# Performance work log

Hardware: AMD Instinct MI355X
Metric: run time of the kernel (lower is better)

The kernel has to match this reference:

```python
import jax, jax.numpy as jnp
import numpy as np

B, F, N = 8, 32, 512
H = 8  # nb_hidden

def setup_inputs() -> dict:
    key = jax.random.key(0)
    ks = jax.random.split(key, 6)
    return {
        "adj_in": jax.random.uniform(ks[0], (B, N, N), dtype=jnp.float32),
        "emb_in": jax.random.normal(ks[1], (B, F, N), dtype=jnp.float32),
        "W1": jax.random.normal(ks[2], (2 * F + 1, H), dtype=jnp.float32) * 0.1,
        "b1": jax.random.normal(ks[3], (H,), dtype=jnp.float32) * 0.1,
        "W2": jax.random.normal(ks[4], (H, 1), dtype=jnp.float32) * 0.1,
        "b2": jax.random.normal(ks[5], (1,), dtype=jnp.float32) * 0.1,
    }

def reference(adj_in, emb_in, W1, b1, W2, b2):
    b_, f_, n_ = emb_in.shape
    # Faithful to the torch code's .resize quirk: column sums always come from
    # batch 0, while the subtracted diagonal is per-batch.
    col_sum0 = adj_in[0].sum(axis=0)                      # [N] = sum_k adj_in[0,k,j]
    diag = jnp.diagonal(adj_in, axis1=1, axis2=2)          # [B,N]
    sw = (col_sum0[None, :] - diag) / (n_ - 1)             # [B,N]
    et = jnp.transpose(emb_in, (0, 2, 1))                  # [B,N,F]
    a = jnp.broadcast_to(et[:, :, None, :], (b_, n_, n_, f_))   # src node i feats
    c = jnp.broadcast_to(et[:, None, :, :], (b_, n_, n_, f_))   # dst node j feats
    swb = jnp.broadcast_to(sw[:, None, :, None], (b_, n_, n_, 1))  # sw[j]
    feat = jnp.concatenate([a, c, swb], axis=-1)           # [B,N,N,2F+1]
    h = jax.nn.relu(feat @ W1 + b1)                        # [B,N,N,H]
    out = (h @ W2 + b2)[..., 0]                            # [B,N,N]
    return jax.nn.sigmoid(out)
```

## Files before the change

### kernel.cpp

```cpp
#include <hip/hip_runtime.h>
#include <math.h>

constexpr int NB = 8;
constexpr int NF = 32;
constexpr int NN = 512;
constexpr int NH = 8;
constexpr int JC = 32;
constexpr int IR = 256;

__global__ __launch_bounds__(512) void fused1_kernel(
    const float* __restrict__ adj, const float* __restrict__ emb,
    const float* __restrict__ W1, const float* __restrict__ b1,
    const float* __restrict__ W2, const float* __restrict__ b2,
    float* __restrict__ out)
{
    __shared__ float u_lds[NH][IR];
    __shared__ float v_lds[NH][JC];
    __shared__ float cs_lds[8][JC];

    const int jc = blockIdx.x;
    const int ih = blockIdx.y;
    const int b  = blockIdx.z;
    const int j0 = jc * JC;
    const int i0 = ih * IR;
    const int t  = threadIdx.x;

    if (t < 256) {
        const int i = i0 + t;
        float uo[NH];
        #pragma unroll
        for (int k = 0; k < NH; ++k) uo[k] = 0.f;
        #pragma unroll 8
        for (int f = 0; f < NF; ++f) {
            const float e = emb[((size_t)b * NF + f) * NN + i];
            #pragma unroll
            for (int k = 0; k < NH; ++k)
                uo[k] = fmaf(e, W1[f * NH + k], uo[k]);
        }
        #pragma unroll
        for (int k = 0; k < NH; ++k) u_lds[k][t] = uo[k];
    } else {
        const int tt = t - 256;
        const int c  = tt & 31;
        const int rg = tt >> 5;
        const float* p = adj + (size_t)(rg * 64) * NN + j0 + c;
        float acc = 0.f;
        #pragma unroll 16
        for (int r = 0; r < 64; ++r)
            acc += p[(size_t)r * NN];
        cs_lds[rg][c] = acc;
    }
    __syncthreads();

    if (t >= 256 && t < 256 + JC) {
        const int c = t - 256;
        const int n = j0 + c;
        float cs = 0.f;
        #pragma unroll
        for (int rg = 0; rg < 8; ++rg) cs += cs_lds[rg][c];
        const float dg = adj[((size_t)b * NN + n) * NN + n];
        const float sw = (cs - dg) * (1.0f / (float)(NN - 1));

        float vo[NH];
        #pragma unroll
        for (int k = 0; k < NH; ++k)
            vo[k] = b1[k] + sw * W1[2 * NF * NH + k];
        #pragma unroll 8
        for (int f = 0; f < NF; ++f) {
            const float e = emb[((size_t)b * NF + f) * NN + n];
            #pragma unroll
            for (int k = 0; k < NH; ++k)
                vo[k] = fmaf(e, W1[(NF + f) * NH + k], vo[k]);
        }
        #pragma unroll
        for (int k = 0; k < NH; ++k) v_lds[k][c] = vo[k];
    }
    __syncthreads();

    float w2[NH];
    #pragma unroll
    for (int k = 0; k < NH; ++k) w2[k] = W2[k];
    const float bias = b2[0];

    const int j    = t & 31;
    const int isub = t >> 5;

    float vv[NH];
    #pragma unroll
    for (int k = 0; k < NH; ++k) vv[k] = v_lds[k][j];

    float* orow = out + ((size_t)b * NN + i0) * NN + j0 + j;
    #pragma unroll 4
    for (int r = 0; r < 16; ++r) {
        const int i = isub * 16 + r;
        float a = bias;
        #pragma unroll
        for (int k = 0; k < NH; ++k)
            a = fmaf(fmaxf(u_lds[k][i] + vv[k], 0.f), w2[k], a);
        orow[(size_t)i * NN] = 1.0f / (1.0f + __expf(-a));
    }
}

extern "C" void kernel_launch(void* const* d_in, const int* in_sizes, int n_in,
                              void* d_out, int out_size, void* d_ws, size_t ws_size,
                              hipStream_t stream) {
    const float* adj = (const float*)d_in[0];
    const float* emb = (const float*)d_in[1];
    const float* W1  = (const float*)d_in[2];
    const float* b1  = (const float*)d_in[3];
    const float* W2  = (const float*)d_in[4];
    const float* b2  = (const float*)d_in[5];
    float* out = (float*)d_out;

    fused1_kernel<<<dim3(NN / JC, NN / IR, NB), 512, 0, stream>>>(
        adj, emb, W1, b1, W2, b2, out);
}
```

Before: 11.84 us.

## Vectorize column-sum loads and output stores with float4, use fast reciprocal

The column-sum phase now has each thread load float4 chunks over 16 rows instead of scalar loads over 64 rows, and keeps 32 partial float4 sums in LDS. The output phase gives each thread 4 consecutive columns and 4 rows, writes float4 stores, and computes the sigmoid with a hardware reciprocal instead of a division. The aim is fewer, wider memory transactions for both the adjacency read and the output write, plus a cheaper sigmoid. The cost is a longer LDS reduction over 32 partials with a select per element, and the fast reciprocal is slightly less accurate.

```diff
diff --git a/kernel.cpp b/kernel.cpp
--- a/kernel.cpp
+++ b/kernel.cpp
@@ -14,9 +14,9 @@
     const float* __restrict__ W2, const float* __restrict__ b2,
     float* __restrict__ out)
 {
-    __shared__ float u_lds[NH][IR];
-    __shared__ float v_lds[NH][JC];
-    __shared__ float cs_lds[8][JC];
+    __shared__ float  u_lds[NH][IR];
+    __shared__ float  v_lds[NH][JC];
+    __shared__ float4 cs_lds[32][8];
 
     const int jc = blockIdx.x;
     const int ih = blockIdx.y;
@@ -41,14 +41,17 @@
         for (int k = 0; k < NH; ++k) u_lds[k][t] = uo[k];
     } else {
         const int tt = t - 256;
-        const int c  = tt & 31;
-        const int rg = tt >> 5;
-        const float* p = adj + (size_t)(rg * 64) * NN + j0 + c;
-        float acc = 0.f;
+        const int c4 = tt & 7;
+        const int rg = tt >> 3;
+        const float4* p = reinterpret_cast<const float4*>(
+            adj + (size_t)(rg * 16) * NN + j0 + c4 * 4);
+        float4 acc = make_float4(0.f, 0.f, 0.f, 0.f);
         #pragma unroll 16
-        for (int r = 0; r < 64; ++r)
-            acc += p[(size_t)r * NN];
-        cs_lds[rg][c] = acc;
+        for (int r = 0; r < 16; ++r) {
+            const float4 x = p[(size_t)r * (NN / 4)];
+            acc.x += x.x; acc.y += x.y; acc.z += x.z; acc.w += x.w;
+        }
+        cs_lds[rg][c4] = acc;
     }
     __syncthreads();
 
@@ -57,7 +60,10 @@
         const int n = j0 + c;
         float cs = 0.f;
         #pragma unroll
-        for (int rg = 0; rg < 8; ++rg) cs += cs_lds[rg][c];
+        for (int rg = 0; rg < 32; ++rg) {
+            const float4 q = cs_lds[rg][c >> 2];
+            cs += (c & 3) == 0 ? q.x : (c & 3) == 1 ? q.y : (c & 3) == 2 ? q.z : q.w;
+        }
         const float dg = adj[((size_t)b * NN + n) * NN + n];
         const float sw = (cs - dg) * (1.0f / (float)(NN - 1));
 
@@ -82,22 +88,33 @@
     for (int k = 0; k < NH; ++k) w2[k] = W2[k];
     const float bias = b2[0];
 
-    const int j    = t & 31;
-    const int isub = t >> 5;
+    const int j4 = (t & 7) * 4;
+    const int ig = t >> 3;
 
-    float vv[NH];
+    float4 vv[NH];
     #pragma unroll
-    for (int k = 0; k < NH; ++k) vv[k] = v_lds[k][j];
+    for (int k = 0; k < NH; ++k)
+        vv[k] = *reinterpret_cast<const float4*>(&v_lds[k][j4]);
 
-    float* orow = out + ((size_t)b * NN + i0) * NN + j0 + j;
-    #pragma unroll 4
-    for (int r = 0; r < 16; ++r) {
-        const int i = isub * 16 + r;
-        float a = bias;
+    float* obase = out + ((size_t)b * NN + i0) * NN + j0 + j4;
+    #pragma unroll
+    for (int r = 0; r < 4; ++r) {
+        const int i = ig * 4 + r;
+        float4 a = make_float4(bias, bias, bias, bias);
         #pragma unroll
-        for (int k = 0; k < NH; ++k)
-            a = fmaf(fmaxf(u_lds[k][i] + vv[k], 0.f), w2[k], a);
-        orow[(size_t)i * NN] = 1.0f / (1.0f + __expf(-a));
+        for (int k = 0; k < NH; ++k) {
+            const float uk = u_lds[k][i];
+            a.x = fmaf(fmaxf(uk + vv[k].x, 0.f), w2[k], a.x);
+            a.y = fmaf(fmaxf(uk + vv[k].y, 0.f), w2[k], a.y);
+            a.z = fmaf(fmaxf(uk + vv[k].z, 0.f), w2[k], a.z);
+            a.w = fmaf(fmaxf(uk + vv[k].w, 0.f), w2[k], a.w);
+        }
+        float4 o;
+        o.x = __builtin_amdgcn_rcpf(1.0f + __expf(-a.x));
+        o.y = __builtin_amdgcn_rcpf(1.0f + __expf(-a.y));
+        o.z = __builtin_amdgcn_rcpf(1.0f + __expf(-a.z));
+        o.w = __builtin_amdgcn_rcpf(1.0f + __expf(-a.w));
+        *reinterpret_cast<float4*>(obase + (size_t)i * NN) = o;
     }
 }
 
```

Result: slower. 13.73 us (+16.0%).
